# Optimization experiments

Hardware: AMD Instinct MI355X
Metric: run time of the kernel (lower is better)

The kernel has to match this reference:

```python
import math
import jax, jax.numpy as jnp
import numpy as np

B, L, D, H = 4, 2048, 1024, 16
DH = D // H  # head dim = 64
PAD_LEN = 128  # trailing padded positions


def setup_inputs() -> dict:
    key = jax.random.key(0)
    ks = jax.random.split(key, 12)
    q = jax.random.normal(ks[0], (B, L, D), dtype=jnp.float32)
    k = jax.random.normal(ks[1], (B, L, D), dtype=jnp.float32)
    v = jax.random.normal(ks[2], (B, L, D), dtype=jnp.float32)
    # additive causal mask: 0 on/below diagonal, -inf above
    causal = jnp.triu(jnp.ones((L, L), dtype=bool), k=1)
    att_mask = jnp.where(causal, -jnp.inf, 0.0).astype(jnp.float32)
    # boolean pad mask over key positions: last PAD_LEN positions are padding
    pad_mask = (jnp.arange(L) >= (L - PAD_LEN))[None, :].repeat(B, axis=0)
    s = 0.02
    params = {
        'w_q': jax.random.normal(ks[3], (D, D), jnp.float32) * s,
        'b_q': jnp.zeros((D,), jnp.float32),
        'w_k': jax.random.normal(ks[4], (D, D), jnp.float32) * s,
        'b_k': jnp.zeros((D,), jnp.float32),
        'w_v': jax.random.normal(ks[5], (D, D), jnp.float32) * s,
        'b_v': jnp.zeros((D,), jnp.float32),
        'w_out': jax.random.normal(ks[6], (D, D), jnp.float32) * s,
        'b_out': jnp.zeros((D,), jnp.float32),
    }
    return {'q': q, 'k': k, 'v': v, 'att_mask': att_mask, 'pad_mask': pad_mask, **params}


def reference(q, k, v, att_mask, pad_mask, w_q, b_q, w_k, b_k, w_v, b_v, w_out, b_out):
    b, l, d = q.shape
    qp = q @ w_q.T + b_q
    kp = k @ w_k.T + b_k  # computed but unused below: source stacks q for k and v (faithful)
    vp = v @ w_v.T + b_v  # computed but unused below (faithful to source bug)
    # split(ndim//nhead, dim=2) + stack(dim=1) == reshape + transpose -> [B,H,L,DH]
    qh = qp.reshape(b, l, H, DH).transpose(0, 2, 1, 3)
    kh = qh  # source: torch.stack(q, ...) used for k
    vh = qh  # source: torch.stack(q, ...) used for v
    att = jnp.einsum('bhqd,bhkd->bhqk', qh, kh) / math.sqrt(DH)
    att = att + att_mask  # broadcast [L,L] over [B,H,L,L]
    # pad_mask [B,L] over keys, broadcast across heads and query positions
    att = jnp.where(pad_mask[:, None, None, :], -jnp.inf, att)
    p = jax.nn.softmax(att, axis=-1)
    o = jnp.einsum('bhqk,bhkd->bhqd', p, vh)
    o = o.transpose(0, 2, 1, 3).reshape(b, l, d)
    return o @ w_out.T + b_out
```

## Files before the change

kernel.cpp:

```cpp
#include <hip/hip_runtime.h>
#include <math.h>


typedef __attribute__((ext_vector_type(8))) short bf16x8;
typedef __attribute__((ext_vector_type(8))) unsigned short u16x8;
typedef __attribute__((ext_vector_type(4))) float f32x4;
typedef __attribute__((ext_vector_type(2))) unsigned int u32x2;

#define MFMA16(a, b, c) __builtin_amdgcn_mfma_f32_16x16x32_bf16(a, b, c, 0, 0, 0)

#define GLDS16(g, l) __builtin_amdgcn_global_load_lds(                        \
    (const __attribute__((address_space(1))) unsigned int*)(g),               \
    (__attribute__((address_space(3))) unsigned int*)(l), 16, 0, 0)

#define SCALE_Q   0.42466092f
#define INV_SCALE 2.3548202f

__device__ __forceinline__ unsigned short f2bf(float f) {
    union { float f; unsigned int u; } x; x.f = f;
    unsigned int u = x.u + 0x7fffu + ((x.u >> 16) & 1u);
    return (unsigned short)(u >> 16);
}

__device__ __forceinline__ unsigned int cvt_pk_bf16(float lo, float hi) {
    unsigned int r;
    asm("v_cvt_pk_bf16_f32 %0, %1, %2" : "=v"(r) : "v"(lo), "v"(hi));
    return r;
}

__global__ __launch_bounds__(256) void cast3_bf16(
    const float* __restrict__ s0, unsigned short* __restrict__ d0,
    const float* __restrict__ s1, unsigned short* __restrict__ d1,
    const float* __restrict__ s2, unsigned short* __restrict__ d2)
{
    const float* s; unsigned short* d; int i;
    int blk = blockIdx.x;
    if (blk < 4096)      { s = s0; d = d0; i = (blk * 256 + threadIdx.x) * 8; }
    else if (blk < 4608) { s = s1; d = d1; i = ((blk - 4096) * 256 + threadIdx.x) * 8; }
    else                 { s = s2; d = d2; i = ((blk - 4608) * 256 + threadIdx.x) * 8; }
    f32x4 a = *(const f32x4*)(s + i);
    f32x4 b = *(const f32x4*)(s + i + 4);
    u16x8 o;
    o[0] = f2bf(a[0]); o[1] = f2bf(a[1]); o[2] = f2bf(a[2]); o[3] = f2bf(a[3]);
    o[4] = f2bf(b[0]); o[5] = f2bf(b[1]); o[6] = f2bf(b[2]); o[7] = f2bf(b[3]);
    *(u16x8*)(d + i) = o;
}

__global__ __launch_bounds__(256) void gemm_bt(
    const unsigned short* __restrict__ A,
    const unsigned short* __restrict__ Bw,
    const float* __restrict__ bias,
    unsigned short* __restrict__ Cbf,
    float* __restrict__ Cf,
    int M, int N, int K, int mode)
{
    __shared__ __align__(16) short lA[2][128 * 64];
    __shared__ __align__(16) short lB[2][128 * 64];
    const int tid = threadIdx.x;
    const int lane = tid & 63, w = tid >> 6;
    const int quad = lane >> 4, l16 = lane & 15;
    const int flat = blockIdx.y * 8 + blockIdx.x;
    const int lf = (flat & 7) * 64 + (flat >> 3);
    const int m0 = (lf >> 3) * 128, n0 = (lf & 7) * 128;
    const int wm = (w >> 1) * 64, wn = (w & 1) * 64;

    const int r8 = lane >> 3;
    const int ch = (lane & 7) ^ r8;
    const unsigned short* Ag = A  + (size_t)(m0 + w * 32 + r8) * K + ch * 8;
    const unsigned short* Bg = Bw + (size_t)(n0 + w * 32 + r8) * K + ch * 8;

    f32x4 acc[4][4];
#pragma unroll
    for (int i = 0; i < 4; ++i)
#pragma unroll
        for (int j = 0; j < 4; ++j) acc[i][j] = (f32x4){0.f, 0.f, 0.f, 0.f};

    auto prefetch = [&](int k0, int buf) {
#pragma unroll
        for (int j = 0; j < 4; ++j) {
            GLDS16(Ag + (size_t)j * 8 * K + k0, &lA[buf][(w * 32 + j * 8) * 64]);
            GLDS16(Bg + (size_t)j * 8 * K + k0, &lB[buf][(w * 32 + j * 8) * 64]);
        }
    };
    auto compute = [&](int buf) {
#pragma unroll
        for (int ks = 0; ks < 2; ++ks) {
            const int kc = (ks << 2) + quad;
            const int sw = (kc ^ (l16 & 7)) * 8;
            bf16x8 af[4], bfr[4];
#pragma unroll
            for (int i = 0; i < 4; ++i)
                af[i] = *(bf16x8*)&lA[buf][(wm + i * 16 + l16) * 64 + sw];
#pragma unroll
            for (int j = 0; j < 4; ++j)
                bfr[j] = *(bf16x8*)&lB[buf][(wn + j * 16 + l16) * 64 + sw];
#pragma unroll
            for (int i = 0; i < 4; ++i)
#pragma unroll
                for (int j = 0; j < 4; ++j)
                    acc[i][j] = MFMA16(af[i], bfr[j], acc[i][j]);
        }
    };

    const int niter = K >> 6;
    prefetch(0, 0);
    for (int k = 0; k < niter; k += 2) {
        __syncthreads();
        if (k + 1 < niter) prefetch((k + 1) << 6, 1);
        compute(0);
        __syncthreads();
        if (k + 2 < niter) prefetch((k + 2) << 6, 0);
        if (k + 1 < niter) compute(1);
    }

#pragma unroll
    for (int i = 0; i < 4; ++i)
#pragma unroll
        for (int j = 0; j < 4; ++j) {
            int col = n0 + wn + j * 16 + l16;
            float bv = bias[col];
#pragma unroll
            for (int r = 0; r < 4; ++r) {
                int row = m0 + wm + i * 16 + quad * 4 + r;
                float v = acc[i][j][r] + bv;
                if (mode == 0) {
                    int b = row >> 11, l = row & 2047;
                    int h = col >> 6, dh = col & 63;
                    Cbf[(((size_t)(b * 16 + h) * 2048) + l) * 64 + dh] = f2bf(v * SCALE_Q);
                } else {
                    Cf[(size_t)row * N + col] = v;
                }
            }
        }
}

__global__ __launch_bounds__(256, 4) void attn_kernel(
    const unsigned short* __restrict__ qh,
    unsigned short* __restrict__ obf)
{
    __shared__ __align__(16) short kvb [2][64 * 64];
    __shared__ __align__(16) short kvtb[2][64 * 64];
    __shared__ __align__(16) short pls [8][16 * 32];
    const int tid = threadIdx.x;
    const int lane = tid & 63, w = tid >> 6;
    const int quad = lane >> 4, l16 = lane & 15;
    const int s7 = l16 & 7, s3 = l16 & 3;
    const int bh = blockIdx.x & 63;
    const int g = blockIdx.x >> 6;
    const int ga = g >> 2, gb = g & 3;
    const int qt2 = (ga == 0) ? 15 - gb : (ga == 1) ? 8 + gb : (ga == 2) ? 7 - gb : gb;
    const int rbase = qt2 << 7;
    const unsigned short* __restrict__ base = qh + ((size_t)bh << 17);

    bf16x8 bq[2][2];
    int rmin[2];
#pragma unroll
    for (int s = 0; s < 2; ++s) {
        rmin[s] = rbase + w * 32 + s * 16;
        const unsigned short* qrow = base + (size_t)(rmin[s] + l16) * 64 + quad * 8;
        bq[s][0] = *(const bf16x8*)qrow;
        bq[s][1] = *(const bf16x8*)(qrow + 32);
    }

    f32x4 oacc[2][4];
    f32x4 sacc[2];
#pragma unroll
    for (int s = 0; s < 2; ++s) {
        sacc[s] = (f32x4){0.f, 0.f, 0.f, 0.f};
#pragma unroll
        for (int t = 0; t < 4; ++t) oacc[s][t] = (f32x4){0.f, 0.f, 0.f, 0.f};
    }

    bf16x8 ones;
#pragma unroll
    for (int j = 0; j < 8; ++j) ones[j] = (short)0x3F80;

    const int nkt = min(2 * qt2 + 2, 30);
    short* pw0 = pls[w * 2 + 0];
    short* pw1 = pls[w * 2 + 1];

    u16x8 d0, d1;
    {
        const unsigned short* src = base + (size_t)lane * 64 + w * 16;
        d0 = *(const u16x8*)src;
        d1 = *(const u16x8*)(src + 8);
        short* kvn = kvb[0]; short* kvtn = kvtb[0];
        *(u16x8*)&kvn[lane * 64 + (((2 * w)     ^ (lane & 7)) * 8)] = d0;
        *(u16x8*)&kvn[lane * 64 + (((2 * w + 1) ^ (lane & 7)) * 8)] = d1;
#pragma unroll
        for (int j = 0; j < 8; ++j) {
            kvtn[(w * 16 + j)     * 64 + (((lane >> 3) ^ j) * 8) + (lane & 7)] = d0[j];
            kvtn[(w * 16 + 8 + j) * 64 + (((lane >> 3) ^ j) * 8) + (lane & 7)] = d1[j];
        }
        const unsigned short* s1 = base + (size_t)(64 + lane) * 64 + w * 16;
        d0 = *(const u16x8*)s1;
        d1 = *(const u16x8*)(s1 + 8);
        __syncthreads();
    }

    auto tile = [&](int kt, bool masked) {
        const int kb = kt << 6;
        const short* kvc  = kvb [kt & 1];
        const short* kvtc = kvtb[kt & 1];
        const bool act0 = !masked || (kb <= rmin[0] + 15);
        const bool act1 = !masked || (kb <= rmin[1] + 15);
        const bool dg0 = masked && (kb + 63 > rmin[0]);
        const bool dg1 = masked && (kb + 63 > rmin[1]);
        __builtin_amdgcn_s_setprio(1);
#pragma unroll
        for (int tp = 0; tp < 2; ++tp) {
#pragma unroll
            for (int th = 0; th < 2; ++th) {
                const int t = tp * 2 + th;
                bf16x8 fk0 = *(bf16x8*)&kvc[(t * 16 + l16) * 64 + ((quad       ^ s7) * 8)];
                bf16x8 fk1 = *(bf16x8*)&kvc[(t * 16 + l16) * 64 + (((quad + 4) ^ s7) * 8)];
                const int keyb = kb + t * 16 + 4 * quad;
                const int goff = ((th * 2 + (quad >> 1)) ^ s3) * 8 + (quad & 1) * 4;
#pragma unroll
                for (int s = 0; s < 2; ++s) {
                    if (masked && !(s ? act1 : act0)) continue;
                    f32x4 sv = (f32x4){0.f, 0.f, 0.f, 0.f};
                    sv = MFMA16(fk0, bq[s][0], sv);
                    sv = MFMA16(fk1, bq[s][1], sv);
                    float p[4];
#pragma unroll
                    for (int r = 0; r < 4; ++r) {
                        float pv = exp2f(sv[r]);
                        if (masked) {
                            const bool dgs = s ? dg1 : dg0;
                            if (dgs && (keyb + r > rmin[s] + l16)) pv = 0.f;
                        }
                        p[r] = pv;
                    }
                    u32x2 pk;
                    pk[0] = cvt_pk_bf16(p[0], p[1]);
                    pk[1] = cvt_pk_bf16(p[2], p[3]);
                    short* pws = s ? pw1 : pw0;
                    *(u32x2*)&pws[l16 * 32 + goff] = pk;
                }
            }
            bf16x8 bp0, bp1;
            const int gr = (quad ^ s3) * 8;
            if (act0) bp0 = *(bf16x8*)&pw0[l16 * 32 + gr];
            if (act1) bp1 = *(bf16x8*)&pw1[l16 * 32 + gr];
            if (act0) sacc[0] = MFMA16(ones, bp0, sacc[0]);
            if (act1) sacc[1] = MFMA16(ones, bp1, sacc[1]);
#pragma unroll
            for (int t2 = 0; t2 < 4; ++t2) {
                bf16x8 av = *(bf16x8*)&kvtc[(t2 * 16 + l16) * 64 + (((tp * 4 + quad) ^ s7) * 8)];
                if (act0) oacc[0][t2] = MFMA16(av, bp0, oacc[0][t2]);
                if (act1) oacc[1][t2] = MFMA16(av, bp1, oacc[1][t2]);
            }
        }
        if (kt + 1 < nkt) {
            const int nxt = (kt & 1) ^ 1;
            short* kvn = kvb[nxt]; short* kvtn = kvtb[nxt];
            *(u16x8*)&kvn[lane * 64 + (((2 * w)     ^ (lane & 7)) * 8)] = d0;
            *(u16x8*)&kvn[lane * 64 + (((2 * w + 1) ^ (lane & 7)) * 8)] = d1;
#pragma unroll
            for (int j = 0; j < 8; ++j) {
                kvtn[(w * 16 + j)     * 64 + (((lane >> 3) ^ j) * 8) + (lane & 7)] = d0[j];
                kvtn[(w * 16 + 8 + j) * 64 + (((lane >> 3) ^ j) * 8) + (lane & 7)] = d1[j];
            }
        }
        if (kt + 2 < nkt) {
            const unsigned short* src = base + (size_t)((kt + 2) * 64 + lane) * 64 + w * 16;
            d0 = *(const u16x8*)src;
            d1 = *(const u16x8*)(src + 8);
        }
        __builtin_amdgcn_s_setprio(0);
        asm volatile("s_waitcnt lgkmcnt(0)" ::: "memory");
        __builtin_amdgcn_s_barrier();
        asm volatile("" ::: "memory");
        __builtin_amdgcn_sched_barrier(0);
    };

    const int ncl = nkt - 2;
    for (int kt = 0; kt < ncl; ++kt) tile(kt, false);
    for (int kt = ncl; kt < nkt; ++kt) tile(kt, true);

    const int b = bh >> 4, h = bh & 15;
#pragma unroll
    for (int s = 0; s < 2; ++s) {
        const float inv = INV_SCALE / sacc[s][0];
        unsigned short* orow = obf + ((size_t)(b * 2048 + rmin[s] + l16)) * 1024
                             + h * 64 + 4 * quad;
#pragma unroll
        for (int t2 = 0; t2 < 4; ++t2) {
            u32x2 pk;
            pk[0] = cvt_pk_bf16(oacc[s][t2][0] * inv, oacc[s][t2][1] * inv);
            pk[1] = cvt_pk_bf16(oacc[s][t2][2] * inv, oacc[s][t2][3] * inv);
            *(u32x2*)(orow + t2 * 16) = pk;
        }
    }
}

extern "C" void kernel_launch(void* const* d_in, const int* in_sizes, int n_in,
                              void* d_out, int out_size, void* d_ws, size_t ws_size,
                              hipStream_t stream) {
    const float* q     = (const float*)d_in[0];
    const float* w_q   = (const float*)d_in[5];
    const float* b_q   = (const float*)d_in[6];
    const float* w_out = (const float*)d_in[11];
    const float* b_out = (const float*)d_in[12];
    float* out = (float*)d_out;

    char* ws = (char*)d_ws;
    unsigned short* a_bf   = (unsigned short*)ws;
    unsigned short* wq_bf  = (unsigned short*)(ws + (16u << 20));
    unsigned short* wo_bf  = (unsigned short*)(ws + (18u << 20));
    unsigned short* qheads = (unsigned short*)(ws + (20u << 20));
    unsigned short* o_bf   = a_bf;

    hipLaunchKernelGGL(cast3_bf16, dim3(5120), dim3(256), 0, stream,
                       q, a_bf, w_q, wq_bf, w_out, wo_bf);

    hipLaunchKernelGGL(gemm_bt, dim3(8, 64), dim3(256), 0, stream,
                       a_bf, wq_bf, b_q, qheads, (float*)nullptr, 8192, 1024, 1024, 0);
    hipLaunchKernelGGL(attn_kernel, dim3(1024), dim3(256), 0, stream, qheads, o_bf);
    hipLaunchKernelGGL(gemm_bt, dim3(8, 64), dim3(256), 0, stream,
                       o_bf, wo_bf, b_out, (unsigned short*)nullptr, out, 8192, 1024, 1024, 1);
}
```

Measured before the change: 260.0 us.

## Pre-transpose Q heads in a separate kernel and load K fragments directly from global

```diff
diff --git a/kernel.cpp b/kernel.cpp
--- a/kernel.cpp
+++ b/kernel.cpp
@@ -134,11 +134,33 @@
         }
 }
 
+__global__ __launch_bounds__(256) void transpose_qh(
+    const unsigned short* __restrict__ qh,
+    unsigned short* __restrict__ qhT)
+{
+    __shared__ short t[64 * 72];
+    const int tid = threadIdx.x;
+    const int bh = blockIdx.y;
+    const int kb = blockIdx.x << 6;
+    const int k = tid >> 2, c = (tid & 3) * 16;
+    const unsigned short* src = qh + ((size_t)bh << 17) + (size_t)(kb + k) * 64 + c;
+    u16x8 a = *(const u16x8*)src;
+    u16x8 b = *(const u16x8*)(src + 8);
+#pragma unroll
+    for (int j = 0; j < 8; ++j) t[(c + j) * 72 + k]     = a[j];
+#pragma unroll
+    for (int j = 0; j < 8; ++j) t[(c + 8 + j) * 72 + k] = b[j];
+    __syncthreads();
+    unsigned short* dst = qhT + ((size_t)bh << 17) + (size_t)k * 2048 + kb + c;
+    *(u16x8*)dst       = *(u16x8*)&t[k * 72 + c];
+    *(u16x8*)(dst + 8) = *(u16x8*)&t[k * 72 + c + 8];
+}
+
 __global__ __launch_bounds__(256, 4) void attn_kernel(
     const unsigned short* __restrict__ qh,
+    const unsigned short* __restrict__ qhT,
     unsigned short* __restrict__ obf)
 {
-    __shared__ __align__(16) short kvb [2][64 * 64];
     __shared__ __align__(16) short kvtb[2][64 * 64];
     __shared__ __align__(16) short pls [8][16 * 32];
     const int tid = threadIdx.x;
@@ -150,7 +172,8 @@
     const int ga = g >> 2, gb = g & 3;
     const int qt2 = (ga == 0) ? 15 - gb : (ga == 1) ? 8 + gb : (ga == 2) ? 7 - gb : gb;
     const int rbase = qt2 << 7;
-    const unsigned short* __restrict__ base = qh + ((size_t)bh << 17);
+    const unsigned short* __restrict__ base  = qh  + ((size_t)bh << 17);
+    const unsigned short* __restrict__ baseT = qhT + ((size_t)bh << 17);
 
     bf16x8 bq[2][2];
     int rmin[2];
@@ -179,49 +202,53 @@
     short* pw0 = pls[w * 2 + 0];
     short* pw1 = pls[w * 2 + 1];
 
-    u16x8 d0, d1;
+    const int sd = w * 16 + (lane >> 2);
+    const int sb = (lane & 3) * 2;
+    const int lds_c0 = sd * 64 + ((sb ^ (sd & 7)) * 8);
+    const int lds_c1 = sd * 64 + (((sb + 1) ^ (sd & 7)) * 8);
+    const unsigned short* tsrc = baseT + (size_t)sd * 2048 + sb * 8;
+
+    u16x8 e0, e1;
     {
-        const unsigned short* src = base + (size_t)lane * 64 + w * 16;
-        d0 = *(const u16x8*)src;
-        d1 = *(const u16x8*)(src + 8);
-        short* kvn = kvb[0]; short* kvtn = kvtb[0];
-        *(u16x8*)&kvn[lane * 64 + (((2 * w)     ^ (lane & 7)) * 8)] = d0;
-        *(u16x8*)&kvn[lane * 64 + (((2 * w + 1) ^ (lane & 7)) * 8)] = d1;
-#pragma unroll
-        for (int j = 0; j < 8; ++j) {
-            kvtn[(w * 16 + j)     * 64 + (((lane >> 3) ^ j) * 8) + (lane & 7)] = d0[j];
-            kvtn[(w * 16 + 8 + j) * 64 + (((lane >> 3) ^ j) * 8) + (lane & 7)] = d1[j];
-        }
-        const unsigned short* s1 = base + (size_t)(64 + lane) * 64 + w * 16;
-        d0 = *(const u16x8*)s1;
-        d1 = *(const u16x8*)(s1 + 8);
+        e0 = *(const u16x8*)tsrc;
+        e1 = *(const u16x8*)(tsrc + 8);
+        short* kt0 = kvtb[0];
+        *(u16x8*)&kt0[lds_c0] = e0;
+        *(u16x8*)&kt0[lds_c1] = e1;
+        e0 = *(const u16x8*)(tsrc + 64);
+        e1 = *(const u16x8*)(tsrc + 64 + 8);
         __syncthreads();
     }
 
     auto tile = [&](int kt, bool masked) {
         const int kb = kt << 6;
-        const short* kvc  = kvb [kt & 1];
         const short* kvtc = kvtb[kt & 1];
         const bool act0 = !masked || (kb <= rmin[0] + 15);
         const bool act1 = !masked || (kb <= rmin[1] + 15);
         const bool dg0 = masked && (kb + 63 > rmin[0]);
         const bool dg1 = masked && (kb + 63 > rmin[1]);
+
+        bf16x8 kf0[4], kf1[4];
+#pragma unroll
+        for (int t = 0; t < 4; ++t) {
+            const unsigned short* kr = base + (size_t)(kb + t * 16 + l16) * 64 + quad * 8;
+            kf0[t] = *(const bf16x8*)kr;
+            kf1[t] = *(const bf16x8*)(kr + 32);
+        }
         __builtin_amdgcn_s_setprio(1);
 #pragma unroll
         for (int tp = 0; tp < 2; ++tp) {
 #pragma unroll
             for (int th = 0; th < 2; ++th) {
                 const int t = tp * 2 + th;
-                bf16x8 fk0 = *(bf16x8*)&kvc[(t * 16 + l16) * 64 + ((quad       ^ s7) * 8)];
-                bf16x8 fk1 = *(bf16x8*)&kvc[(t * 16 + l16) * 64 + (((quad + 4) ^ s7) * 8)];
                 const int keyb = kb + t * 16 + 4 * quad;
                 const int goff = ((th * 2 + (quad >> 1)) ^ s3) * 8 + (quad & 1) * 4;
 #pragma unroll
                 for (int s = 0; s < 2; ++s) {
                     if (masked && !(s ? act1 : act0)) continue;
                     f32x4 sv = (f32x4){0.f, 0.f, 0.f, 0.f};
-                    sv = MFMA16(fk0, bq[s][0], sv);
-                    sv = MFMA16(fk1, bq[s][1], sv);
+                    sv = MFMA16(kf0[t], bq[s][0], sv);
+                    sv = MFMA16(kf1[t], bq[s][1], sv);
                     float p[4];
 #pragma unroll
                     for (int r = 0; r < 4; ++r) {
@@ -253,20 +280,14 @@
             }
         }
         if (kt + 1 < nkt) {
-            const int nxt = (kt & 1) ^ 1;
-            short* kvn = kvb[nxt]; short* kvtn = kvtb[nxt];
-            *(u16x8*)&kvn[lane * 64 + (((2 * w)     ^ (lane & 7)) * 8)] = d0;
-            *(u16x8*)&kvn[lane * 64 + (((2 * w + 1) ^ (lane & 7)) * 8)] = d1;
-#pragma unroll
-            for (int j = 0; j < 8; ++j) {
-                kvtn[(w * 16 + j)     * 64 + (((lane >> 3) ^ j) * 8) + (lane & 7)] = d0[j];
-                kvtn[(w * 16 + 8 + j) * 64 + (((lane >> 3) ^ j) * 8) + (lane & 7)] = d1[j];
-            }
+            short* ktn = kvtb[(kt & 1) ^ 1];
+            *(u16x8*)&ktn[lds_c0] = e0;
+            *(u16x8*)&ktn[lds_c1] = e1;
         }
         if (kt + 2 < nkt) {
-            const unsigned short* src = base + (size_t)((kt + 2) * 64 + lane) * 64 + w * 16;
-            d0 = *(const u16x8*)src;
-            d1 = *(const u16x8*)(src + 8);
+            const unsigned short* ts = tsrc + (kt + 2) * 64;
+            e0 = *(const u16x8*)ts;
+            e1 = *(const u16x8*)(ts + 8);
         }
         __builtin_amdgcn_s_setprio(0);
         asm volatile("s_waitcnt lgkmcnt(0)" ::: "memory");
@@ -310,6 +331,7 @@
     unsigned short* wq_bf  = (unsigned short*)(ws + (16u << 20));
     unsigned short* wo_bf  = (unsigned short*)(ws + (18u << 20));
     unsigned short* qheads = (unsigned short*)(ws + (20u << 20));
+    unsigned short* qhT    = (unsigned short*)(ws + (36u << 20));
     unsigned short* o_bf   = a_bf;
 
     hipLaunchKernelGGL(cast3_bf16, dim3(5120), dim3(256), 0, stream,
@@ -317,7 +339,8 @@
 
     hipLaunchKernelGGL(gemm_bt, dim3(8, 64), dim3(256), 0, stream,
                        a_bf, wq_bf, b_q, qheads, (float*)nullptr, 8192, 1024, 1024, 0);
-    hipLaunchKernelGGL(attn_kernel, dim3(1024), dim3(256), 0, stream, qheads, o_bf);
+    hipLaunchKernelGGL(transpose_qh, dim3(32, 64), dim3(256), 0, stream, qheads, qhT);
+    hipLaunchKernelGGL(attn_kernel, dim3(1024), dim3(256), 0, stream, qheads, qhT, o_bf);
     hipLaunchKernelGGL(gemm_bt, dim3(8, 64), dim3(256), 0, stream,
                        o_bf, wo_bf, b_out, (unsigned short*)nullptr, out, 8192, 1024, 1024, 1);
 }
```

Measured after the change: 292.1 us. 12.3% more time.

## Emit transposed Q heads from projection GEMM to avoid LDS transpose in attention

Applied to the files above, without the earlier changes.

```diff
diff --git a/kernel.cpp b/kernel.cpp
--- a/kernel.cpp
+++ b/kernel.cpp
@@ -51,6 +51,7 @@
     const unsigned short* __restrict__ Bw,
     const float* __restrict__ bias,
     unsigned short* __restrict__ Cbf,
+    unsigned short* __restrict__ CbT,
     float* __restrict__ Cf,
     int M, int N, int K, int mode)
 {
@@ -119,16 +120,26 @@
         for (int j = 0; j < 4; ++j) {
             int col = n0 + wn + j * 16 + l16;
             float bv = bias[col];
-#pragma unroll
-            for (int r = 0; r < 4; ++r) {
-                int row = m0 + wm + i * 16 + quad * 4 + r;
-                float v = acc[i][j][r] + bv;
-                if (mode == 0) {
-                    int b = row >> 11, l = row & 2047;
-                    int h = col >> 6, dh = col & 63;
-                    Cbf[(((size_t)(b * 16 + h) * 2048) + l) * 64 + dh] = f2bf(v * SCALE_Q);
-                } else {
-                    Cf[(size_t)row * N + col] = v;
+            if (mode == 0) {
+                const int row0 = m0 + wm + i * 16 + quad * 4;
+                const int b = row0 >> 11, l0 = row0 & 2047;
+                const int h = col >> 6, dh = col & 63;
+                float v[4];
+#pragma unroll
+                for (int r = 0; r < 4; ++r)
+                    v[r] = (acc[i][j][r] + bv) * SCALE_Q;
+#pragma unroll
+                for (int r = 0; r < 4; ++r)
+                    Cbf[(((size_t)(b * 16 + h) * 2048) + l0 + r) * 64 + dh] = f2bf(v[r]);
+                u32x2 pk;
+                pk[0] = cvt_pk_bf16(v[0], v[1]);
+                pk[1] = cvt_pk_bf16(v[2], v[3]);
+                *(u32x2*)&CbT[((size_t)(b * 16 + h) * 64 + dh) * 2048 + l0] = pk;
+            } else {
+#pragma unroll
+                for (int r = 0; r < 4; ++r) {
+                    int row = m0 + wm + i * 16 + quad * 4 + r;
+                    Cf[(size_t)row * N + col] = acc[i][j][r] + bv;
                 }
             }
         }
@@ -136,6 +147,7 @@
 
 __global__ __launch_bounds__(256, 4) void attn_kernel(
     const unsigned short* __restrict__ qh,
+    const unsigned short* __restrict__ qhT,
     unsigned short* __restrict__ obf)
 {
     __shared__ __align__(16) short kvb [2][64 * 64];
@@ -150,7 +162,8 @@
     const int ga = g >> 2, gb = g & 3;
     const int qt2 = (ga == 0) ? 15 - gb : (ga == 1) ? 8 + gb : (ga == 2) ? 7 - gb : gb;
     const int rbase = qt2 << 7;
-    const unsigned short* __restrict__ base = qh + ((size_t)bh << 17);
+    const unsigned short* __restrict__ base  = qh  + ((size_t)bh << 17);
+    const unsigned short* __restrict__ baseT = qhT + ((size_t)bh << 17);
 
     bf16x8 bq[2][2];
     int rmin[2];
@@ -179,22 +192,29 @@
     short* pw0 = pls[w * 2 + 0];
     short* pw1 = pls[w * 2 + 1];
 
-    u16x8 d0, d1;
+    const unsigned short* ksrc = base + (size_t)lane * 64 + w * 16;
+    const int kv_c0 = lane * 64 + (((2 * w)     ^ (lane & 7)) * 8);
+    const int kv_c1 = lane * 64 + (((2 * w + 1) ^ (lane & 7)) * 8);
+    const int sd = w * 16 + (lane >> 2);
+    const int sb = (lane & 3) * 2;
+    const int kt_c0 = sd * 64 + ((sb ^ (sd & 7)) * 8);
+    const int kt_c1 = sd * 64 + (((sb + 1) ^ (sd & 7)) * 8);
+    const unsigned short* tsrc = baseT + (size_t)sd * 2048 + sb * 8;
+
+    u16x8 d0, d1, e0, e1;
     {
-        const unsigned short* src = base + (size_t)lane * 64 + w * 16;
-        d0 = *(const u16x8*)src;
-        d1 = *(const u16x8*)(src + 8);
-        short* kvn = kvb[0]; short* kvtn = kvtb[0];
-        *(u16x8*)&kvn[lane * 64 + (((2 * w)     ^ (lane & 7)) * 8)] = d0;
-        *(u16x8*)&kvn[lane * 64 + (((2 * w + 1) ^ (lane & 7)) * 8)] = d1;
-#pragma unroll
-        for (int j = 0; j < 8; ++j) {
-            kvtn[(w * 16 + j)     * 64 + (((lane >> 3) ^ j) * 8) + (lane & 7)] = d0[j];
-            kvtn[(w * 16 + 8 + j) * 64 + (((lane >> 3) ^ j) * 8) + (lane & 7)] = d1[j];
-        }
-        const unsigned short* s1 = base + (size_t)(64 + lane) * 64 + w * 16;
-        d0 = *(const u16x8*)s1;
-        d1 = *(const u16x8*)(s1 + 8);
+        d0 = *(const u16x8*)ksrc;
+        d1 = *(const u16x8*)(ksrc + 8);
+        e0 = *(const u16x8*)tsrc;
+        e1 = *(const u16x8*)(tsrc + 8);
+        *(u16x8*)&kvb [0][kv_c0] = d0;
+        *(u16x8*)&kvb [0][kv_c1] = d1;
+        *(u16x8*)&kvtb[0][kt_c0] = e0;
+        *(u16x8*)&kvtb[0][kt_c1] = e1;
+        d0 = *(const u16x8*)(ksrc + 64 * 64);
+        d1 = *(const u16x8*)(ksrc + 64 * 64 + 8);
+        e0 = *(const u16x8*)(tsrc + 64);
+        e1 = *(const u16x8*)(tsrc + 64 + 8);
         __syncthreads();
     }
 
@@ -254,19 +274,18 @@
         }
         if (kt + 1 < nkt) {
             const int nxt = (kt & 1) ^ 1;
-            short* kvn = kvb[nxt]; short* kvtn = kvtb[nxt];
-            *(u16x8*)&kvn[lane * 64 + (((2 * w)     ^ (lane & 7)) * 8)] = d0;
-            *(u16x8*)&kvn[lane * 64 + (((2 * w + 1) ^ (lane & 7)) * 8)] = d1;
-#pragma unroll
-            for (int j = 0; j < 8; ++j) {
-                kvtn[(w * 16 + j)     * 64 + (((lane >> 3) ^ j) * 8) + (lane & 7)] = d0[j];
-                kvtn[(w * 16 + 8 + j) * 64 + (((lane >> 3) ^ j) * 8) + (lane & 7)] = d1[j];
-            }
+            *(u16x8*)&kvb [nxt][kv_c0] = d0;
+            *(u16x8*)&kvb [nxt][kv_c1] = d1;
+            *(u16x8*)&kvtb[nxt][kt_c0] = e0;
+            *(u16x8*)&kvtb[nxt][kt_c1] = e1;
         }
         if (kt + 2 < nkt) {
-            const unsigned short* src = base + (size_t)((kt + 2) * 64 + lane) * 64 + w * 16;
-            d0 = *(const u16x8*)src;
-            d1 = *(const u16x8*)(src + 8);
+            const unsigned short* ks2 = ksrc + (size_t)(kt + 2) * 64 * 64;
+            const unsigned short* ts2 = tsrc + (kt + 2) * 64;
+            d0 = *(const u16x8*)ks2;
+            d1 = *(const u16x8*)(ks2 + 8);
+            e0 = *(const u16x8*)ts2;
+            e1 = *(const u16x8*)(ts2 + 8);
         }
         __builtin_amdgcn_s_setprio(0);
         asm volatile("s_waitcnt lgkmcnt(0)" ::: "memory");
@@ -310,14 +329,16 @@
     unsigned short* wq_bf  = (unsigned short*)(ws + (16u << 20));
     unsigned short* wo_bf  = (unsigned short*)(ws + (18u << 20));
     unsigned short* qheads = (unsigned short*)(ws + (20u << 20));
+    unsigned short* qhT    = (unsigned short*)(ws + (36u << 20));
     unsigned short* o_bf   = a_bf;
 
     hipLaunchKernelGGL(cast3_bf16, dim3(5120), dim3(256), 0, stream,
                        q, a_bf, w_q, wq_bf, w_out, wo_bf);
 
     hipLaunchKernelGGL(gemm_bt, dim3(8, 64), dim3(256), 0, stream,
-                       a_bf, wq_bf, b_q, qheads, (float*)nullptr, 8192, 1024, 1024, 0);
-    hipLaunchKernelGGL(attn_kernel, dim3(1024), dim3(256), 0, stream, qheads, o_bf);
+                       a_bf, wq_bf, b_q, qheads, qhT, (float*)nullptr, 8192, 1024, 1024, 0);
+    hipLaunchKernelGGL(attn_kernel, dim3(1024), dim3(256), 0, stream, qheads, qhT, o_bf);
     hipLaunchKernelGGL(gemm_bt, dim3(8, 64), dim3(256), 0, stream,
-                       o_bf, wo_bf, b_out, (unsigned short*)nullptr, out, 8192, 1024, 1024, 1);
-}
+                       o_bf, wo_bf, b_out, (unsigned short*)nullptr, (unsigned short*)nullptr,
+                       out, 8192, 1024, 1024, 1);
+}
```

New measurement: 263.1 us. About the same (+1.2%).
